# Kernel optimization log

Hardware: AMD Instinct MI355X
Metric: run time of the kernel (lower is better)

The kernel has to match this reference:

```python
import jax, jax.numpy as jnp
import numpy as np

NF, NV = 400000, 200000
C_IN, C_OUT, K, MULT = 64, 128, 27, 1
BN_EPS = 1e-5


def setup_inputs() -> dict:
    key = jax.random.key(0)
    ks = jax.random.split(key, 8)
    inputs = jax.random.normal(ks[0], (NF, C_IN), dtype=jnp.float32)
    filt_coeff = jax.random.uniform(ks[1], (NF, K), dtype=jnp.float32)
    face = jax.random.randint(ks[2], (NF, 3), 0, NV, dtype=jnp.int32)
    nf_count = jnp.ones((NV,), dtype=jnp.int32)
    vt_map = jnp.arange(NV, dtype=jnp.int64)
    # learned parameters (xavier-ish scale)
    spatial_weights = jax.random.normal(ks[3], (K, C_IN, MULT), dtype=jnp.float32) * np.sqrt(2.0 / (K * C_IN + MULT))
    depth_weights = jax.random.normal(ks[4], (C_IN * MULT, C_OUT), dtype=jnp.float32) * np.sqrt(2.0 / (C_IN * MULT + C_OUT))
    biases = jnp.zeros((1, C_OUT), dtype=jnp.float32)
    gamma = jnp.ones((C_OUT,), dtype=jnp.float32)
    beta = jnp.zeros((C_OUT,), dtype=jnp.float32)
    return {
        "inputs": inputs, "filt_coeff": filt_coeff, "face": face,
        "nf_count": nf_count, "vt_map": vt_map,
        "spatial_weights": spatial_weights, "depth_weights": depth_weights,
        "biases": biases, "gamma": gamma, "beta": beta,
    }


def reference(inputs, filt_coeff, face, nf_count, vt_map,
              spatial_weights, depth_weights, biases, gamma, beta):
    nv = nf_count.shape[0]
    nf = inputs.shape[0]
    # per-face mixture of spatial filters: [Nf, C_in, mult]
    w = jnp.einsum('fk,kcm->fcm', filt_coeff, spatial_weights)
    # per-face weighted features, flattened depthwise: [Nf, C_in*mult]
    contrib = (inputs[:, :, None] * w).reshape(nf, -1)
    # scatter each face's contribution to its 3 vertices
    idx = face.reshape(-1)                                  # [3*Nf]
    vals = jnp.broadcast_to(contrib[:, None, :], (nf, 3, contrib.shape[1])).reshape(3 * nf, -1)
    agg = jax.ops.segment_sum(vals, idx, num_segments=nv)    # [Nv, C_in*mult]
    # average by number of adjacent faces
    denom = jnp.maximum(nf_count, 1).astype(agg.dtype)[:, None]
    agg = agg / denom
    # reorder vertices per vt_map
    agg = agg[vt_map]
    # pointwise (depth) conv + bias + ReLU
    out = agg @ depth_weights + biases
    out = jax.nn.relu(out)
    # BatchNorm1d (training-mode batch statistics over vertices)
    mean = out.mean(axis=0)
    var = out.var(axis=0)
    out = (out - mean) * jax.lax.rsqrt(var + BN_EPS) * gamma + beta
    return out
```

## Files before the change

kernel.cpp:

```cpp
#include <hip/hip_runtime.h>
#include <hip/hip_bf16.h>

#define NFACE 400000
#define NVERT 200000
#define CIN 64
#define COUT 128
#define KF 27
#define BN_EPS 1e-5f

#define M_TOT (NFACE * 3)
#define NB    391
#define NBLK  256
#define CHUNK ((M_TOT + NBLK - 1) / NBLK)

typedef __attribute__((ext_vector_type(8))) short bf16x8;
typedef __attribute__((ext_vector_type(4))) float f32x4;

__device__ __forceinline__ short f2bf(float x) {
    __hip_bfloat16 h = __float2bfloat16(x);
    return *reinterpret_cast<short*>(&h);
}
__device__ __forceinline__ float bf2f(unsigned short u) {
    union { unsigned int i; float f; } x; x.i = ((unsigned)u) << 16; return x.f;
}

__global__ __launch_bounds__(256) void prep_k(const float* __restrict__ sw,
                                              const float* __restrict__ dw,
                                              short* __restrict__ swf,
                                              short* __restrict__ dwb) {
    int t = threadIdx.x;
    {
        int cb = t >> 6, lane = t & 63;
        int ch = cb * 16 + (lane & 15);
#pragma unroll
        for (int j = 0; j < 8; ++j) {
            int k = (lane >> 4) * 8 + j;
            swf[t * 8 + j] = (k < KF) ? f2bf(sw[k * 64 + ch]) : (short)0;
        }
    }
#pragma unroll
    for (int p4 = 0; p4 < 4; ++p4) {
        int p = t + p4 * 256;
        int frag = p >> 6, lane = p & 63;
        int nb = frag >> 3, tt = (frag >> 1) & 3, kk = frag & 1;
        int col = nb * 64 + tt * 16 + (lane & 15);
#pragma unroll
        for (int j = 0; j < 8; ++j) {
            int k = kk * 32 + (lane >> 4) * 8 + j;
            dwb[(size_t)p * 8 + j] = f2bf(dw[k * 128 + col]);
        }
    }
}

__global__ __launch_bounds__(256) void hist_k(const int* __restrict__ faceflat,
                                              int* __restrict__ blockcnt) {
    __shared__ int h[512];
    const int t = threadIdx.x, blk = blockIdx.x;
    for (int j = t; j < 512; j += 256) h[j] = 0;
    __syncthreads();
    int e0 = blk * CHUNK;
    int e1 = min(e0 + CHUNK, M_TOT);
    for (int e = e0 + t; e < e1; e += 256)
        atomicAdd(&h[faceflat[e] >> 9], 1);
    __syncthreads();
    for (int j = t; j < 512; j += 256) blockcnt[blk * 512 + j] = h[j];
}

__global__ __launch_bounds__(256) void scan_k(int* __restrict__ blockcnt,
                                              int* __restrict__ bucket_start,
                                              int* __restrict__ row_off) {
    __shared__ int tot[512];
    __shared__ int bst[512];
    const int t = threadIdx.x;
    for (int b = t; b < 512; b += 256) {
        int acc = 0;
        if (b < NB)
            for (int k = 0; k < NBLK; ++k) acc += blockcnt[k * 512 + b];
        tot[b] = acc;
    }
    __syncthreads();
    if (t < 64) {
        int base8 = t * 8, loc[8], s = 0;
#pragma unroll
        for (int j = 0; j < 8; ++j) { loc[j] = s; s += tot[base8 + j]; }
        int v = s;
        for (int off = 1; off < 64; off <<= 1) {
            int u = __shfl_up(v, off);
            if (t >= off) v += u;
        }
        int excl = v - s;
#pragma unroll
        for (int j = 0; j < 8; ++j) bst[base8 + j] = excl + loc[j];
    }
    __syncthreads();
    for (int b = t; b < NB; b += 256) bucket_start[b] = bst[b];
    if (t == 0) { bucket_start[NB] = bst[NB]; row_off[NVERT] = M_TOT; }
    for (int b = t; b < NB; b += 256) {
        int acc = bst[b];
        for (int k = 0; k < NBLK; ++k) {
            int c = blockcnt[k * 512 + b];
            blockcnt[k * 512 + b] = acc;
            acc += c;
        }
    }
}

__global__ __launch_bounds__(256) void scat_k(const int* __restrict__ faceflat,
                                              const int* __restrict__ blockcnt,
                                              int2* __restrict__ pairs) {
    __shared__ int baseL[512];
    __shared__ int lc[512];
    const int t = threadIdx.x, blk = blockIdx.x;
    for (int j = t; j < 512; j += 256) { baseL[j] = blockcnt[blk * 512 + j]; lc[j] = 0; }
    __syncthreads();
    int e0 = blk * CHUNK;
    int e1 = min(e0 + CHUNK, M_TOT);
    for (int e = e0 + t; e < e1; e += 256) {
        int v = faceflat[e];
        int b = v >> 9;
        int l = atomicAdd(&lc[b], 1);
        pairs[baseL[b] + l] = make_int2(v, e / 3);
    }
}

__global__ __launch_bounds__(256) void csr_k(const int2* __restrict__ pairs,
                                             const int* __restrict__ bucket_start,
                                             int* __restrict__ row_off,
                                             int* __restrict__ csr) {
    __shared__ int cnt[512], esc[512], pc[512];
    const int t = threadIdx.x, b = blockIdx.x;
    const int p0 = bucket_start[b], p1 = bucket_start[b + 1];
    const int vbase = b << 9;
    for (int j = t; j < 512; j += 256) { cnt[j] = 0; pc[j] = 0; }
    __syncthreads();
    for (int i = p0 + t; i < p1; i += 256)
        atomicAdd(&cnt[pairs[i].x - vbase], 1);
    __syncthreads();
    if (t < 64) {
        int base8 = t * 8, loc[8], s = 0;
#pragma unroll
        for (int j = 0; j < 8; ++j) { loc[j] = s; s += cnt[base8 + j]; }
        int v = s;
        for (int off = 1; off < 64; off <<= 1) {
            int u = __shfl_up(v, off);
            if (t >= off) v += u;
        }
        int excl = v - s;
#pragma unroll
        for (int j = 0; j < 8; ++j) esc[base8 + j] = excl + loc[j];
    }
    __syncthreads();
    int nvb = min(512, NVERT - vbase);
    for (int j = t; j < nvb; j += 256) row_off[vbase + j] = p0 + esc[j];
    for (int i = p0 + t; i < p1; i += 256) {
        int lv = pairs[i].x - vbase;
        int l = atomicAdd(&pc[lv], 1);
        csr[p0 + esc[lv] + l] = pairs[i].y;
    }
}

__global__ __launch_bounds__(256) void mix_k(
    const float* __restrict__ inputs,
    const float* __restrict__ filt,
    const short* __restrict__ swf,
    __hip_bfloat16* __restrict__ contrib)
{
    const int t    = threadIdx.x;
    const int lane = t & 63;
    const int wid  = t >> 6;
    const int fb   = blockIdx.x * 64;
    const int f    = fb + wid * 16 + (lane & 15);
    const int qg   = lane >> 4;

    bf16x8 afr[4];
#pragma unroll
    for (int cb = 0; cb < 4; ++cb)
        afr[cb] = *(const bf16x8*)&swf[(cb * 64 + lane) * 8];

    int k0 = qg * 8;
    size_t base = (size_t)f * KF + k0;
    const size_t lim = (size_t)NFACE * KF - 8;
    bool cl = base > lim;
    if (cl) base = lim;
    float4 fa  = *(const float4*)&filt[base];
    float4 fb4 = *(const float4*)&filt[base + 4];
    float wv[8] = {fa.x, fa.y, fa.z, fa.w, fb4.x, fb4.y, fb4.z, fb4.w};
    bf16x8 b;
#pragma unroll
    for (int j = 0; j < 8; ++j) {
        int k = k0 + j;
        float val = cl ? ((j < 3) ? wv[j + 5] : 0.f)
                       : ((k < KF) ? wv[j] : 0.f);
        b[j] = f2bf(val);
    }

    f32x4 acc[4];
#pragma unroll
    for (int cb = 0; cb < 4; ++cb)
        acc[cb] = __builtin_amdgcn_mfma_f32_16x16x32_bf16(afr[cb], b, (f32x4){0.f, 0.f, 0.f, 0.f}, 0, 0, 0);

#pragma unroll
    for (int cb = 0; cb < 4; ++cb) {
        int c0 = cb * 16 + qg * 4;
        float4 in4 = *(const float4*)&inputs[(size_t)f * 64 + c0];
        short4 o;
        o.x = f2bf(in4.x * acc[cb][0]);
        o.y = f2bf(in4.y * acc[cb][1]);
        o.z = f2bf(in4.z * acc[cb][2]);
        o.w = f2bf(in4.w * acc[cb][3]);
        *(short4*)((short*)contrib + (size_t)f * 64 + c0) = o;
    }
}

#define BV 32
__global__ __launch_bounds__(256, 6) void pconv_k(
    const __hip_bfloat16* __restrict__ contrib,
    const int* __restrict__ row_off,
    const int* __restrict__ csr,
    const int* __restrict__ nf_count,
    const int* __restrict__ vt_map,
    const short* __restrict__ dwb,
    const float* __restrict__ bias,
    __hip_bfloat16* __restrict__ outb,
    float* __restrict__ stats)
{
    __shared__ float denL[BV];
    __shared__ int   offL[BV];
    __shared__ int   degL[BV];
    __shared__ int   flatL[BV][32];
    __shared__ __align__(16) short A[BV * 64];
    __shared__ __align__(16) short outL[BV * 128];

    const int t     = threadIdx.x;
    const int lane  = t & 63;
    const int wid   = t >> 6;
    const int vbase = blockIdx.x * BV;
    const unsigned short* ct = (const unsigned short*)contrib;

    if (t < BV) {
        int src = vt_map[vbase + t];
        denL[t] = 1.f / (float)max(nf_count[src], 1);
        int o = row_off[src];
        int d = row_off[src + 1] - o;
        offL[t] = o;
        degL[t] = d > 32 ? 32 : d;
    }
    __syncthreads();
#pragma unroll
    for (int r = 0; r < 4; ++r) {
        int i = t + r * 256;
        int row = i >> 5, j = i & 31;
        flatL[row][j] = (j < degL[row]) ? csr[offL[row] + j] : 0;
    }
    __syncthreads();

#pragma unroll
    for (int g = 0; g < 2; ++g) {
        const int q0 = wid * 8 + g * 4;
        const int n0 = degL[q0 + 0], n1 = degL[q0 + 1];
        const int n2 = degL[q0 + 2], n3 = degL[q0 + 3];
        int jm = max(max(n0, n1), max(n2, n3));
        float s0 = 0.f, s1 = 0.f, s2 = 0.f, s3 = 0.f;
        for (int j = 0; j < jm; j += 4) {
            int f00 = flatL[q0 + 0][j + 0], f01 = flatL[q0 + 0][j + 1];
            int f02 = flatL[q0 + 0][j + 2], f03 = flatL[q0 + 0][j + 3];
            int f10 = flatL[q0 + 1][j + 0], f11 = flatL[q0 + 1][j + 1];
            int f12 = flatL[q0 + 1][j + 2], f13 = flatL[q0 + 1][j + 3];
            int f20 = flatL[q0 + 2][j + 0], f21 = flatL[q0 + 2][j + 1];
            int f22 = flatL[q0 + 2][j + 2], f23 = flatL[q0 + 2][j + 3];
            int f30 = flatL[q0 + 3][j + 0], f31 = flatL[q0 + 3][j + 1];
            int f32_ = flatL[q0 + 3][j + 2], f33 = flatL[q0 + 3][j + 3];
            float v00 = bf2f(ct[(size_t)f00 * 64 + lane]);
            float v01 = bf2f(ct[(size_t)f01 * 64 + lane]);
            float v02 = bf2f(ct[(size_t)f02 * 64 + lane]);
            float v03 = bf2f(ct[(size_t)f03 * 64 + lane]);
            float v10 = bf2f(ct[(size_t)f10 * 64 + lane]);
            float v11 = bf2f(ct[(size_t)f11 * 64 + lane]);
            float v12 = bf2f(ct[(size_t)f12 * 64 + lane]);
            float v13 = bf2f(ct[(size_t)f13 * 64 + lane]);
            float v20 = bf2f(ct[(size_t)f20 * 64 + lane]);
            float v21 = bf2f(ct[(size_t)f21 * 64 + lane]);
            float v22 = bf2f(ct[(size_t)f22 * 64 + lane]);
            float v23 = bf2f(ct[(size_t)f23 * 64 + lane]);
            float v30 = bf2f(ct[(size_t)f30 * 64 + lane]);
            float v31 = bf2f(ct[(size_t)f31 * 64 + lane]);
            float v32 = bf2f(ct[(size_t)f32_ * 64 + lane]);
            float v33 = bf2f(ct[(size_t)f33 * 64 + lane]);
            s0 += ((j + 0 < n0) ? v00 : 0.f) + ((j + 1 < n0) ? v01 : 0.f)
                + ((j + 2 < n0) ? v02 : 0.f) + ((j + 3 < n0) ? v03 : 0.f);
            s1 += ((j + 0 < n1) ? v10 : 0.f) + ((j + 1 < n1) ? v11 : 0.f)
                + ((j + 2 < n1) ? v12 : 0.f) + ((j + 3 < n1) ? v13 : 0.f);
            s2 += ((j + 0 < n2) ? v20 : 0.f) + ((j + 1 < n2) ? v21 : 0.f)
                + ((j + 2 < n2) ? v22 : 0.f) + ((j + 3 < n2) ? v23 : 0.f);
            s3 += ((j + 0 < n3) ? v30 : 0.f) + ((j + 1 < n3) ? v31 : 0.f)
                + ((j + 2 < n3) ? v32 : 0.f) + ((j + 3 < n3) ? v33 : 0.f);
        }
        s0 *= denL[q0 + 0]; s1 *= denL[q0 + 1];
        s2 *= denL[q0 + 2]; s3 *= denL[q0 + 3];
#pragma unroll
        for (int r = 0; r < 4; ++r) {
            int q = q0 + r;
            float sv = (r == 0) ? s0 : (r == 1) ? s1 : (r == 2) ? s2 : s3;
            int swz = (lane & 7) | ((((lane >> 3) ^ (q & 7))) << 3);
            A[q * 64 + swz] = f2bf(sv);
        }
    }
    __syncthreads();

    const int mi = wid & 1;
    const int nbq = wid >> 1;
    f32x4 acc[4];
#pragma unroll
    for (int tt = 0; tt < 4; ++tt) acc[tt] = (f32x4){0.f, 0.f, 0.f, 0.f};
#pragma unroll
    for (int kk = 0; kk < 2; ++kk) {
        int row = mi * 16 + (lane & 15);
        int chunk = (kk * 4 + (lane >> 4)) ^ (row & 7);
        bf16x8 a = *(const bf16x8*)&A[row * 64 + chunk * 8];
#pragma unroll
        for (int tt = 0; tt < 4; ++tt) {
            int frag = (nbq * 4 + tt) * 2 + kk;
            bf16x8 b = *(const bf16x8*)&dwb[((size_t)frag * 64 + lane) * 8];
            acc[tt] = __builtin_amdgcn_mfma_f32_16x16x32_bf16(a, b, acc[tt], 0, 0, 0);
        }
    }

    float* st = stats + (blockIdx.x & 7) * 256;
#pragma unroll
    for (int tt = 0; tt < 4; ++tt) {
        int col = nbq * 64 + tt * 16 + (lane & 15);
        float bv = bias[col];
        float s = 0.f, s2 = 0.f;
#pragma unroll
        for (int i = 0; i < 4; ++i) {
            float o = fmaxf(acc[tt][i] + bv, 0.f);
            int row = mi * 16 + (lane >> 4) * 4 + i;
            outL[row * 128 + col] = f2bf(o);
            s  += o;
            s2 += o * o;
        }
        s  += __shfl_xor(s, 16);  s  += __shfl_xor(s, 32);
        s2 += __shfl_xor(s2, 16); s2 += __shfl_xor(s2, 32);
        if ((lane >> 4) == 0) {
            atomicAdd(&st[col], s);
            atomicAdd(&st[128 + col], s2);
        }
    }
    __syncthreads();

#pragma unroll
    for (int r = 0; r < 2; ++r) {
        int i = t + r * 256;
        ((int4*)&outb[(size_t)vbase * 128])[i] = ((const int4*)outL)[i];
    }
}

__global__ __launch_bounds__(256) void bn_k(
    const __hip_bfloat16* __restrict__ outb,
    float* __restrict__ out,
    const float* __restrict__ stats,
    const float* __restrict__ gamma,
    const float* __restrict__ beta)
{
    __shared__ float sc[128], sh[128];
    if (threadIdx.x < 128) {
        int c = threadIdx.x;
        float s = 0.f, s2 = 0.f;
#pragma unroll
        for (int r = 0; r < 8; ++r) {
            s  += stats[r * 256 + c];
            s2 += stats[r * 256 + 128 + c];
        }
        float mean = s / (float)NVERT;
        float var  = s2 / (float)NVERT - mean * mean;
        float inv  = rsqrtf(var + BN_EPS) * gamma[c];
        sc[c] = inv;
        sh[c] = beta[c] - mean * inv;
    }
    __syncthreads();

    const unsigned short* ob = (const unsigned short*)outb;
    float4* o4 = (float4*)out;
    size_t total4 = (size_t)NVERT * COUT / 4;
    for (size_t i = (size_t)blockIdx.x * 256 + threadIdx.x; i < total4;
         i += (size_t)gridDim.x * 256) {
        int c0 = (int)((i * 4) & 127);
        ushort4 u = *(const ushort4*)&ob[i * 4];
        float4 v;
        v.x = bf2f(u.x) * sc[c0 + 0] + sh[c0 + 0];
        v.y = bf2f(u.y) * sc[c0 + 1] + sh[c0 + 1];
        v.z = bf2f(u.z) * sc[c0 + 2] + sh[c0 + 2];
        v.w = bf2f(u.w) * sc[c0 + 3] + sh[c0 + 3];
        o4[i] = v;
    }
}

extern "C" void kernel_launch(void* const* d_in, const int* in_sizes, int n_in,
                              void* d_out, int out_size, void* d_ws, size_t ws_size,
                              hipStream_t stream) {
    const float* inputs   = (const float*)d_in[0];
    const float* filt     = (const float*)d_in[1];
    const int*   face     = (const int*)d_in[2];
    const int*   nf_count = (const int*)d_in[3];
    const int*   vt_map   = (const int*)d_in[4];
    const float* sw       = (const float*)d_in[5];
    const float* dw       = (const float*)d_in[6];
    const float* bias     = (const float*)d_in[7];
    const float* gamma    = (const float*)d_in[8];
    const float* beta     = (const float*)d_in[9];
    float* out = (float*)d_out;

    char* w = (char*)d_ws;
    float*          stats = (float*)w;
    short*          swf   = (short*)(w + 8192);
    short*          dwb   = (short*)(w + 16384);
    __hip_bfloat16* outb  = (__hip_bfloat16*)(w + 32768);

    char* o = (char*)d_out;
    __hip_bfloat16* contrib      = (__hip_bfloat16*)o;
    int2*           pairs        = (int2*)(o + 51200000);
    int*            csr          = (int*)(o + 60800000);
    int*            row_off      = (int*)(o + 65600000);
    int*            blockcnt     = (int*)(o + 66400256);
    int*            bucket_start = (int*)(o + 66924544);
    const int*      faceflat     = face;

    hipMemsetAsync(stats, 0, 8192, stream);

    prep_k<<<1, 256, 0, stream>>>(sw, dw, swf, dwb);
    hist_k<<<NBLK, 256, 0, stream>>>(faceflat, blockcnt);
    scan_k<<<1, 256, 0, stream>>>(blockcnt, bucket_start, row_off);
    scat_k<<<NBLK, 256, 0, stream>>>(faceflat, blockcnt, pairs);
    csr_k<<<NB, 256, 0, stream>>>(pairs, bucket_start, row_off, csr);
    mix_k<<<NFACE / 64, 256, 0, stream>>>(inputs, filt, swf, contrib);
    pconv_k<<<NVERT / BV, 256, 0, stream>>>(contrib, row_off, csr, nf_count,
                                            vt_map, dwb, bias, outb, stats);
    bn_k<<<2048, 256, 0, stream>>>(outb, out, stats, gamma, beta);
}
```

Before: 193.5 us.

## Merge prep, memset and histogram launches; widen BN stores with nontemporal hints

Folds the stats memset, the weight-prep kernel and the histogram kernel into one launch, with block 0 doing the prep and zeroing. It adds nontemporal loads in the mix kernel for streamed inputs and filter coefficients. The BN kernel now handles 8 elements per thread with nontemporal stores and runs with twice the grid size. The aim is to cut launch overhead and cache pollution, at the cost of a serial prep block inside the histogram launch.

```diff
diff --git a/kernel.cpp b/kernel.cpp
--- a/kernel.cpp
+++ b/kernel.cpp
@@ -15,6 +15,7 @@
 
 typedef __attribute__((ext_vector_type(8))) short bf16x8;
 typedef __attribute__((ext_vector_type(4))) float f32x4;
+typedef __attribute__((ext_vector_type(8))) unsigned short ushort8;
 
 __device__ __forceinline__ short f2bf(float x) {
     __hip_bfloat16 h = __float2bfloat16(x);
@@ -24,46 +25,48 @@
     union { unsigned int i; float f; } x; x.i = ((unsigned)u) << 16; return x.f;
 }
 
-__global__ __launch_bounds__(256) void prep_k(const float* __restrict__ sw,
-                                              const float* __restrict__ dw,
-                                              short* __restrict__ swf,
-                                              short* __restrict__ dwb) {
-    int t = threadIdx.x;
-    {
-        int cb = t >> 6, lane = t & 63;
-        int ch = cb * 16 + (lane & 15);
-#pragma unroll
-        for (int j = 0; j < 8; ++j) {
-            int k = (lane >> 4) * 8 + j;
-            swf[t * 8 + j] = (k < KF) ? f2bf(sw[k * 64 + ch]) : (short)0;
-        }
-    }
-#pragma unroll
-    for (int p4 = 0; p4 < 4; ++p4) {
-        int p = t + p4 * 256;
-        int frag = p >> 6, lane = p & 63;
-        int nb = frag >> 3, tt = (frag >> 1) & 3, kk = frag & 1;
-        int col = nb * 64 + tt * 16 + (lane & 15);
-#pragma unroll
-        for (int j = 0; j < 8; ++j) {
-            int k = kk * 32 + (lane >> 4) * 8 + j;
-            dwb[(size_t)p * 8 + j] = f2bf(dw[k * 128 + col]);
-        }
-    }
-}
-
-__global__ __launch_bounds__(256) void hist_k(const int* __restrict__ faceflat,
-                                              int* __restrict__ blockcnt) {
-    __shared__ int h[512];
-    const int t = threadIdx.x, blk = blockIdx.x;
-    for (int j = t; j < 512; j += 256) h[j] = 0;
-    __syncthreads();
-    int e0 = blk * CHUNK;
-    int e1 = min(e0 + CHUNK, M_TOT);
-    for (int e = e0 + t; e < e1; e += 256)
-        atomicAdd(&h[faceflat[e] >> 9], 1);
-    __syncthreads();
-    for (int j = t; j < 512; j += 256) blockcnt[blk * 512 + j] = h[j];
+__global__ __launch_bounds__(256) void prep_hist_k(
+    const float* __restrict__ sw, const float* __restrict__ dw,
+    short* __restrict__ swf, short* __restrict__ dwb,
+    float* __restrict__ stats,
+    const int* __restrict__ faceflat, int* __restrict__ blockcnt) {
+    const int t = threadIdx.x;
+    if (blockIdx.x == 0) {
+#pragma unroll
+        for (int j = 0; j < 8; ++j) stats[t + j * 256] = 0.f;
+        {
+            int cb = t >> 6, lane = t & 63;
+            int ch = cb * 16 + (lane & 15);
+#pragma unroll
+            for (int j = 0; j < 8; ++j) {
+                int k = (lane >> 4) * 8 + j;
+                swf[t * 8 + j] = (k < KF) ? f2bf(sw[k * 64 + ch]) : (short)0;
+            }
+        }
+#pragma unroll
+        for (int p4 = 0; p4 < 4; ++p4) {
+            int p = t + p4 * 256;
+            int frag = p >> 6, lane = p & 63;
+            int nb = frag >> 3, tt = (frag >> 1) & 3, kk = frag & 1;
+            int col = nb * 64 + tt * 16 + (lane & 15);
+#pragma unroll
+            for (int j = 0; j < 8; ++j) {
+                int k = kk * 32 + (lane >> 4) * 8 + j;
+                dwb[(size_t)p * 8 + j] = f2bf(dw[k * 128 + col]);
+            }
+        }
+    } else {
+        __shared__ int h[512];
+        const int blk = blockIdx.x - 1;
+        for (int j = t; j < 512; j += 256) h[j] = 0;
+        __syncthreads();
+        int e0 = blk * CHUNK;
+        int e1 = min(e0 + CHUNK, M_TOT);
+        for (int e = e0 + t; e < e1; e += 256)
+            atomicAdd(&h[faceflat[e] >> 9], 1);
+        __syncthreads();
+        for (int j = t; j < 512; j += 256) blockcnt[blk * 512 + j] = h[j];
+    }
 }
 
 __global__ __launch_bounds__(256) void scan_k(int* __restrict__ blockcnt,
@@ -182,9 +185,9 @@
     const size_t lim = (size_t)NFACE * KF - 8;
     bool cl = base > lim;
     if (cl) base = lim;
-    float4 fa  = *(const float4*)&filt[base];
-    float4 fb4 = *(const float4*)&filt[base + 4];
-    float wv[8] = {fa.x, fa.y, fa.z, fa.w, fb4.x, fb4.y, fb4.z, fb4.w};
+    f32x4 fa  = __builtin_nontemporal_load((const f32x4*)&filt[base]);
+    f32x4 fb4 = __builtin_nontemporal_load((const f32x4*)&filt[base + 4]);
+    float wv[8] = {fa[0], fa[1], fa[2], fa[3], fb4[0], fb4[1], fb4[2], fb4[3]};
     bf16x8 b;
 #pragma unroll
     for (int j = 0; j < 8; ++j) {
@@ -202,12 +205,13 @@
 #pragma unroll
     for (int cb = 0; cb < 4; ++cb) {
         int c0 = cb * 16 + qg * 4;
-        float4 in4 = *(const float4*)&inputs[(size_t)f * 64 + c0];
+        f32x4 in4 = __builtin_nontemporal_load(
+            (const f32x4*)&inputs[(size_t)f * 64 + c0]);
         short4 o;
-        o.x = f2bf(in4.x * acc[cb][0]);
-        o.y = f2bf(in4.y * acc[cb][1]);
-        o.z = f2bf(in4.z * acc[cb][2]);
-        o.w = f2bf(in4.w * acc[cb][3]);
+        o.x = f2bf(in4[0] * acc[cb][0]);
+        o.y = f2bf(in4[1] * acc[cb][1]);
+        o.z = f2bf(in4[2] * acc[cb][2]);
+        o.w = f2bf(in4[3] * acc[cb][3]);
         *(short4*)((short*)contrib + (size_t)f * 64 + c0) = o;
     }
 }
@@ -379,19 +383,23 @@
     }
     __syncthreads();
 
-    const unsigned short* ob = (const unsigned short*)outb;
-    float4* o4 = (float4*)out;
-    size_t total4 = (size_t)NVERT * COUT / 4;
-    for (size_t i = (size_t)blockIdx.x * 256 + threadIdx.x; i < total4;
+    const ushort8* ob8 = (const ushort8*)outb;
+    size_t total8 = (size_t)NVERT * COUT / 8;
+    for (size_t i = (size_t)blockIdx.x * 256 + threadIdx.x; i < total8;
          i += (size_t)gridDim.x * 256) {
-        int c0 = (int)((i * 4) & 127);
-        ushort4 u = *(const ushort4*)&ob[i * 4];
-        float4 v;
-        v.x = bf2f(u.x) * sc[c0 + 0] + sh[c0 + 0];
-        v.y = bf2f(u.y) * sc[c0 + 1] + sh[c0 + 1];
-        v.z = bf2f(u.z) * sc[c0 + 2] + sh[c0 + 2];
-        v.w = bf2f(u.w) * sc[c0 + 3] + sh[c0 + 3];
-        o4[i] = v;
+        int c0 = (int)((i * 8) & 127);
+        ushort8 u = ob8[i];
+        f32x4 v0, v1;
+        v0[0] = bf2f(u[0]) * sc[c0 + 0] + sh[c0 + 0];
+        v0[1] = bf2f(u[1]) * sc[c0 + 1] + sh[c0 + 1];
+        v0[2] = bf2f(u[2]) * sc[c0 + 2] + sh[c0 + 2];
+        v0[3] = bf2f(u[3]) * sc[c0 + 3] + sh[c0 + 3];
+        v1[0] = bf2f(u[4]) * sc[c0 + 4] + sh[c0 + 4];
+        v1[1] = bf2f(u[5]) * sc[c0 + 5] + sh[c0 + 5];
+        v1[2] = bf2f(u[6]) * sc[c0 + 6] + sh[c0 + 6];
+        v1[3] = bf2f(u[7]) * sc[c0 + 7] + sh[c0 + 7];
+        __builtin_nontemporal_store(v0, (f32x4*)&out[i * 8]);
+        __builtin_nontemporal_store(v1, (f32x4*)&out[i * 8 + 4]);
     }
 }
 
@@ -425,15 +433,13 @@
     int*            bucket_start = (int*)(o + 66924544);
     const int*      faceflat     = face;
 
-    hipMemsetAsync(stats, 0, 8192, stream);
-
-    prep_k<<<1, 256, 0, stream>>>(sw, dw, swf, dwb);
-    hist_k<<<NBLK, 256, 0, stream>>>(faceflat, blockcnt);
+    prep_hist_k<<<NBLK + 1, 256, 0, stream>>>(sw, dw, swf, dwb, stats,
+                                              faceflat, blockcnt);
     scan_k<<<1, 256, 0, stream>>>(blockcnt, bucket_start, row_off);
     scat_k<<<NBLK, 256, 0, stream>>>(faceflat, blockcnt, pairs);
     csr_k<<<NB, 256, 0, stream>>>(pairs, bucket_start, row_off, csr);
     mix_k<<<NFACE / 64, 256, 0, stream>>>(inputs, filt, swf, contrib);
     pconv_k<<<NVERT / BV, 256, 0, stream>>>(contrib, row_off, csr, nf_count,
                                             vt_map, dwb, bias, outb, stats);
-    bn_k<<<2048, 256, 0, stream>>>(outb, out, stats, gamma, beta);
-}
+    bn_k<<<4096, 256, 0, stream>>>(outb, out, stats, gamma, beta);
+}
```

New measurement: 188.9 us, median of 2. 2.4% less time.
